# Kernel tuning notes

Hardware: AMD Instinct MI355X
Metric: run time of the kernel (lower is better)

## Reference

```python
import jax, jax.numpy as jnp
import numpy as np

LEAKY_SLOPE = 0.2
LN_EPS = 1e-5
SOFTMAX_EPS = 1e-16  # PyG softmax denominator eps


def setup_inputs() -> dict:
    key = jax.random.key(0)
    ks = jax.random.split(key, 8)
    N, E, F, H, C, ED = 100000, 1600000, 64, 8, 8, 16
    s = 1.0 / np.sqrt(F)
    return {
        "x": jax.random.normal(ks[0], (N, F), jnp.float32),
        "edge_index": jax.random.randint(ks[1], (2, E), 0, N, jnp.int32),
        "edge_attr": jax.random.normal(ks[2], (E, ED), jnp.float32),
        "W_l": jax.random.normal(ks[3], (H * C, F), jnp.float32) * s,
        "b_l": jnp.zeros((H * C,), jnp.float32),
        "W_r": jax.random.normal(ks[4], (H * C, F), jnp.float32) * s,
        "b_r": jnp.zeros((H * C,), jnp.float32),
        "W_e": jax.random.normal(ks[5], (H * C, ED), jnp.float32) * (1.0 / np.sqrt(ED)),
        "att": jax.random.normal(ks[6], (1, H, C), jnp.float32) * (1.0 / np.sqrt(C)),
        "bias": jnp.zeros((H * C,), jnp.float32),
        "gamma": jnp.ones((F,), jnp.float32),
        "beta": jnp.zeros((F,), jnp.float32),
    }


def reference(x, edge_index, edge_attr, W_l, b_l, W_r, b_r, W_e, att, bias, gamma, beta):
    N, F = x.shape
    H, C = att.shape[1], att.shape[2]
    src, dst = edge_index[0], edge_index[1]  # PyG: row0=source(j), row1=target(i)

    xl = (x @ W_l.T + b_l).reshape(N, H, C)   # lin_l -> x_j side
    xr = (x @ W_r.T + b_r).reshape(N, H, C)   # lin_r -> x_i side
    e = (edge_attr @ W_e.T).reshape(-1, H, C)  # lin_edge (no bias)

    m = jax.nn.leaky_relu(xl[src] + xr[dst] + e, LEAKY_SLOPE)  # [E,H,C]
    logits = jnp.einsum('ehc,hc->eh', m, att[0])               # [E,H]

    # per-destination segment softmax
    mx = jax.ops.segment_max(logits, dst, num_segments=N)      # [N,H]
    mx = jnp.where(jnp.isfinite(mx), mx, 0.0)                  # nodes w/o in-edges
    ex = jnp.exp(logits - mx[dst])
    denom = jax.ops.segment_sum(ex, dst, num_segments=N)
    alpha = ex / (denom[dst] + SOFTMAX_EPS)                    # [E,H]; dropout is identity in eval

    agg = jax.ops.segment_sum(alpha[:, :, None] * xl[src], dst, num_segments=N)  # [N,H,C]
    out = agg.reshape(N, H * C) + bias

    h = out + x  # residual
    mu = jnp.mean(h, axis=-1, keepdims=True)
    var = jnp.mean((h - mu) ** 2, axis=-1, keepdims=True)
    hn = (h - mu) * jax.lax.rsqrt(var + LN_EPS) * gamma + beta
    return jax.nn.relu(hn)
```

## Files before the change

kernel.cpp:

```cpp
#include <hip/hip_runtime.h>

#define LEAKY 0.2f
#define LN_EPS 1e-5f
#define SM_EPS 1e-16f
#define CAP 64
#define WPAD 68

#define BIN_SHIFT 8
#define MAXBINS   448
#define CHUNK_A   7168
#define BCAP      4608
#define EMASK     0x1FFFFF

__global__ __launch_bounds__(256) void k_node_linear(
    const float* __restrict__ x,
    const float* __restrict__ Wl,
    const float* __restrict__ bl,
    const float* __restrict__ Wr,
    const float* __restrict__ br,
    float* __restrict__ xl, float* __restrict__ xr, int N)
{
    __shared__ __align__(16) float sW[64 * WPAD];

    const int tid = threadIdx.x;
    const int side = blockIdx.x & 1;
    const float* __restrict__ W  = side ? Wr : Wl;
    const float* __restrict__ bv = side ? br : bl;
    float* __restrict__ dst      = side ? xr : xl;

    for (int i = tid; i < 4096; i += 256)
        sW[(i >> 6) * WPAD + (i & 63)] = W[i];
    __syncthreads();

    const int lane = tid & 63;
    float4 wq[16];
    #pragma unroll
    for (int q = 0; q < 16; ++q)
        wq[q] = *(const float4*)&sW[lane * WPAD + q * 4];
    const float bb = bv[lane];

    const int stream0 = (blockIdx.x >> 1) * 4 + (tid >> 6);
    const int nstream = (gridDim.x >> 1) * 4;
    for (int n = stream0; n < N; n += nstream) {
        const float4* xrow = (const float4*)(x + (long long)n * 64);
        float a = bb;
        #pragma unroll
        for (int q = 0; q < 16; ++q) {
            const float4 xv = xrow[q];
            const float4 w  = wq[q];
            a = fmaf(xv.x, w.x, fmaf(xv.y, w.y, fmaf(xv.z, w.z, fmaf(xv.w, w.w, a))));
        }
        dst[(long long)n * 64 + lane] = a;
    }
}

__global__ __launch_bounds__(256) void k_bucket(
    const int* __restrict__ ei, int* __restrict__ deg,
    int2* __restrict__ slot2, int E)
{
    const int e = blockIdx.x * 256 + threadIdx.x;
    if (e >= E) return;
    const int dst = ei[E + e];
    const int pos = atomicAdd(deg + dst, 1);
    if (pos < CAP) slot2[(long long)dst * CAP + pos] = make_int2(e, ei[e]);
}

__global__ __launch_bounds__(256) void k_binA(
    const int* __restrict__ ei,
    int* __restrict__ binCnt,
    int2* __restrict__ binArr,
    int E, int nbins)
{
    __shared__ int2 ord[CHUNK_A];
    __shared__ int cnt[MAXBINS], offs[MAXBINS], cur[MAXBINS], resB[MAXBINS];

    const int tid  = threadIdx.x;
    const int lane = tid & 63;
    const int ebase = blockIdx.x * CHUNK_A;
    const int nE = (E - ebase < CHUNK_A) ? (E - ebase) : CHUNK_A;
    const int* __restrict__ dstp = ei + E + ebase;
    const int* __restrict__ srcp = ei + ebase;

    for (int b = tid; b < MAXBINS; b += 256) { cnt[b] = 0; cur[b] = 0; }
    __syncthreads();

    for (int i = tid; i < nE; i += 256)
        atomicAdd(&cnt[dstp[i] >> BIN_SHIFT], 1);
    __syncthreads();

    if (tid < 64) {
        int carry = 0;
        #pragma unroll
        for (int seg = 0; seg < MAXBINS / 64; ++seg) {
            const int v = cnt[seg * 64 + lane];
            int s = v;
            #pragma unroll
            for (int off = 1; off < 64; off <<= 1) {
                const int t = __shfl_up(s, off, 64);
                if (lane >= off) s += t;
            }
            offs[seg * 64 + lane] = carry + s - v;
            carry += __shfl(s, 63, 64);
        }
    }
    __syncthreads();

    for (int i = tid; i < nE; i += 256) {
        const int d = dstp[i];
        const int b = d >> BIN_SHIFT;
        const int pos = atomicAdd(&cur[b], 1);
        ord[offs[b] + pos] =
            make_int2((ebase + i) | ((d & ((1 << BIN_SHIFT) - 1)) << 21), srcp[i]);
    }
    __syncthreads();

    for (int b = tid; b < nbins; b += 256) {
        const int c = cnt[b];
        resB[b] = c ? atomicAdd(&binCnt[b], c) : 0;
    }
    __syncthreads();

    const int wv = tid >> 6;
    for (int b = wv; b < nbins; b += 4) {
        const int c = cnt[b], o = offs[b], r = resB[b];
        for (int k = lane; k < c; k += 64) {
            const int kk = r + k;
            if (kk < BCAP) binArr[(long long)b * BCAP + kk] = ord[o + k];
        }
    }
}

__global__ __launch_bounds__(256) void k_binB(
    const int* __restrict__ binCnt,
    const int2* __restrict__ binArr,
    int* __restrict__ deg,
    int2* __restrict__ slot2,
    int N)
{
    __shared__ int2 ord2[BCAP];
    __shared__ int cnt2[256], offs2[256], cur2[256];

    const int b = blockIdx.x;
    const int tid  = threadIdx.x;
    const int lane = tid & 63;
    const int dst0 = b << BIN_SHIFT;
    int nb = binCnt[b];
    if (nb > BCAP) nb = BCAP;
    const int2* __restrict__ src = binArr + (long long)b * BCAP;

    cnt2[tid] = 0; cur2[tid] = 0;
    __syncthreads();

    for (int i = tid; i < nb; i += 256)
        atomicAdd(&cnt2[((unsigned)src[i].x >> 21) & 0xFF], 1);
    __syncthreads();

    if (tid < 64) {
        int carry = 0;
        #pragma unroll
        for (int seg = 0; seg < 4; ++seg) {
            const int v = cnt2[seg * 64 + lane];
            int s = v;
            #pragma unroll
            for (int off = 1; off < 64; off <<= 1) {
                const int t = __shfl_up(s, off, 64);
                if (lane >= off) s += t;
            }
            offs2[seg * 64 + lane] = carry + s - v;
            carry += __shfl(s, 63, 64);
        }
    }
    __syncthreads();

    for (int i = tid; i < nb; i += 256) {
        const int2 p = src[i];
        const int d = ((unsigned)p.x >> 21) & 0xFF;
        const int pos = atomicAdd(&cur2[d], 1);
        ord2[offs2[d] + pos] = make_int2(p.x & EMASK, p.y);
    }
    __syncthreads();

    const int nd = (N - dst0 < 256) ? (N - dst0) : 256;
    if (tid < nd) deg[dst0 + tid] = cnt2[tid];

    const int wv = tid >> 6;
    for (int d = wv; d < nd; d += 4) {
        int c = cnt2[d];
        if (c > CAP) c = CAP;
        if (lane < c) slot2[(long long)(dst0 + d) * CAP + lane] = ord2[offs2[d] + lane];
    }
}

__global__ __launch_bounds__(256) void k_gather(
    const float* __restrict__ ea,
    const float* __restrict__ We,
    const float* __restrict__ att,
    const float* __restrict__ xl, const float* __restrict__ xr,
    const int* __restrict__ deg, const int2* __restrict__ slot2,
    const float* __restrict__ x,
    const float* __restrict__ bias, const float* __restrict__ gamma,
    const float* __restrict__ beta,
    float* __restrict__ out, int N)
{
    const int lane = threadIdx.x & 63;
    const int n = blockIdx.x * 4 + (threadIdx.x >> 6);
    if (n >= N) return;

    const float4* w4 = (const float4*)(We + lane * 16);
    const float4 w0 = w4[0], w1 = w4[1], w2 = w4[2], w3 = w4[3];
    const float attv = att[lane];
    const float xrv = xr[(long long)n * 64 + lane];

    const int d = min(deg[n], CAP);

    int veid = 0, vsrc = 0;
    if (lane < d) {
        const int2 es = slot2[(long long)n * CAP + lane];
        veid = es.x;
        vsrc = es.y;
    }

    float acc = 0.f;
    float ns  = 0.f;

    float xlA = 0.f, xlB = 0.f;
    float4 a0, a1, a2, a3, b0, b1, b2, b3;
    a0 = a1 = a2 = a3 = b0 = b1 = b2 = b3 = make_float4(0.f, 0.f, 0.f, 0.f);

#define FETCH(j, XLV, E0, E1, E2, E3) do {                       \
        const int s_ = __shfl(vsrc, (j), 64);                    \
        const int e_ = __shfl(veid, (j), 64);                    \
        XLV = xl[(long long)s_ * 64 + lane];                     \
        const float4* p_ = (const float4*)(ea + (long long)e_ * 16); \
        E0 = p_[0]; E1 = p_[1]; E2 = p_[2]; E3 = p_[3];          \
    } while (0)

#define COMPUTE(XLV, E0, E1, E2, E3) do {                        \
        float ep = E0.x*w0.x + E0.y*w0.y + E0.z*w0.z + E0.w*w0.w \
                 + E1.x*w1.x + E1.y*w1.y + E1.z*w1.z + E1.w*w1.w \
                 + E2.x*w2.x + E2.y*w2.y + E2.z*w2.z + E2.w*w2.w \
                 + E3.x*w3.x + E3.y*w3.y + E3.z*w3.z + E3.w*w3.w;\
        float m = XLV + xrv + ep;                                \
        m = (m > 0.f) ? m : LEAKY * m;           \
        float p = m * attv;                                      \
        p += __shfl_xor(p, 1, 64);                               \
        p += __shfl_xor(p, 2, 64);                               \
        p += __shfl_xor(p, 4, 64);                               \
        const float ex = __expf(p);                              \
        ns  += ex;                                               \
        acc = fmaf(ex, XLV, acc);                                \
    } while (0)

    if (d > 0) FETCH(0, xlA, a0, a1, a2, a3);
    if (d > 1) FETCH(1, xlB, b0, b1, b2, b3);

    for (int i = 0; i < d; i += 2) {
        COMPUTE(xlA, a0, a1, a2, a3);
        if (i + 2 < d) FETCH(i + 2, xlA, a0, a1, a2, a3);
        if (i + 1 < d) {
            COMPUTE(xlB, b0, b1, b2, b3);
            if (i + 3 < d) FETCH(i + 3, xlB, b0, b1, b2, b3);
        }
    }
#undef FETCH
#undef COMPUTE

    const float a = acc / (ns + SM_EPS);
    const float hv = a + bias[lane] + x[(long long)n * 64 + lane];

    float s = hv;
    #pragma unroll
    for (int off = 32; off; off >>= 1) s += __shfl_xor(s, off, 64);
    const float mu = s * (1.f / 64.f);
    const float dd = hv - mu;
    float v = dd * dd;
    #pragma unroll
    for (int off = 32; off; off >>= 1) v += __shfl_xor(v, off, 64);
    const float var = v * (1.f / 64.f);

    float hn = dd * rsqrtf(var + LN_EPS) * gamma[lane] + beta[lane];
    out[(long long)n * 64 + lane] = (hn > 0.f) ? hn : 0.f;
}

extern "C" void kernel_launch(void* const* d_in, const int* in_sizes, int n_in,
                              void* d_out, int out_size, void* d_ws, size_t ws_size,
                              hipStream_t stream) {
    (void)n_in; (void)out_size;

    const float* x     = (const float*)d_in[0];
    const int*   ei    = (const int*)d_in[1];
    const float* ea    = (const float*)d_in[2];
    const float* Wl    = (const float*)d_in[3];
    const float* bl    = (const float*)d_in[4];
    const float* Wr    = (const float*)d_in[5];
    const float* br    = (const float*)d_in[6];
    const float* We    = (const float*)d_in[7];
    const float* att   = (const float*)d_in[8];
    const float* bias  = (const float*)d_in[9];
    const float* gamma = (const float*)d_in[10];
    const float* beta  = (const float*)d_in[11];

    const int N = in_sizes[0] / 64;
    const int E = in_sizes[1] / 2;
    const int nbins = (N + (1 << BIN_SHIFT) - 1) >> BIN_SHIFT;

    float* w = (float*)d_ws;
    float* xl   = w;                      w += (size_t)N * 64;
    float* xr   = w;                      w += (size_t)N * 64;
    int* deg    = (int*)w;
    int* binCnt = deg + N;
    int2* slot2 = (int2*)(binCnt + MAXBINS);
    int2* binArr = slot2 + (size_t)N * CAP;
    const size_t needed = ((char*)(binArr + (size_t)nbins * BCAP)) - (char*)d_ws;

    float* out = (float*)d_out;

    const bool binned = (nbins <= MAXBINS) && (E <= (1 << 21)) &&
                        (ws_size >= needed);

    hipMemsetAsync(deg, 0, ((size_t)N + MAXBINS) * sizeof(int), stream);

    k_node_linear<<<2048, 256, 0, stream>>>(x, Wl, bl, Wr, br, xl, xr, N);

    if (binned) {
        const int nbA = (E + CHUNK_A - 1) / CHUNK_A;
        k_binA<<<nbA, 256, 0, stream>>>(ei, binCnt, binArr, E, nbins);
        k_binB<<<nbins, 256, 0, stream>>>(binCnt, binArr, deg, slot2, N);
    } else {
        k_bucket<<<(E + 255) / 256, 256, 0, stream>>>(ei, deg, slot2, E);
    }

    k_gather<<<(N + 3) / 4, 256, 0, stream>>>(
        ea, We, att, xl, xr, deg, slot2, x, bias, gamma, beta, out, N);
}
```

Measured before the change: 645.9 us.

## Process four nodes per wavefront in gather and flatten bin scatter loop

```diff
diff --git a/kernel.cpp b/kernel.cpp
--- a/kernel.cpp
+++ b/kernel.cpp
@@ -8,9 +8,10 @@
 
 #define BIN_SHIFT 8
 #define MAXBINS   448
-#define CHUNK_A   7168
+#define CHUNK_A   5632
 #define BCAP      4608
 #define EMASK     0x1FFFFF
+#define NPW       4
 
 __global__ __launch_bounds__(256) void k_node_linear(
     const float* __restrict__ x,
@@ -72,6 +73,7 @@
     int E, int nbins)
 {
     __shared__ int2 ord[CHUNK_A];
+    __shared__ unsigned short ordBin[CHUNK_A];
     __shared__ int cnt[MAXBINS], offs[MAXBINS], cur[MAXBINS], resB[MAXBINS];
 
     const int tid  = threadIdx.x;
@@ -109,8 +111,9 @@
         const int d = dstp[i];
         const int b = d >> BIN_SHIFT;
         const int pos = atomicAdd(&cur[b], 1);
-        ord[offs[b] + pos] =
-            make_int2((ebase + i) | ((d & ((1 << BIN_SHIFT) - 1)) << 21), srcp[i]);
+        const int at = offs[b] + pos;
+        ord[at] = make_int2((ebase + i) | ((d & ((1 << BIN_SHIFT) - 1)) << 21), srcp[i]);
+        ordBin[at] = (unsigned short)b;
     }
     __syncthreads();
 
@@ -120,13 +123,10 @@
     }
     __syncthreads();
 
-    const int wv = tid >> 6;
-    for (int b = wv; b < nbins; b += 4) {
-        const int c = cnt[b], o = offs[b], r = resB[b];
-        for (int k = lane; k < c; k += 64) {
-            const int kk = r + k;
-            if (kk < BCAP) binArr[(long long)b * BCAP + kk] = ord[o + k];
-        }
+    for (int i = tid; i < nE; i += 256) {
+        const int b = ordBin[i];
+        const int k = resB[b] + (i - offs[b]);
+        if (k < BCAP) binArr[(long long)b * BCAP + k] = ord[i];
     }
 }
 
@@ -203,33 +203,41 @@
     float* __restrict__ out, int N)
 {
     const int lane = threadIdx.x & 63;
-    const int n = blockIdx.x * 4 + (threadIdx.x >> 6);
-    if (n >= N) return;
+    const int wid  = blockIdx.x * 4 + (threadIdx.x >> 6);
+    const int n0   = wid * NPW;
+    if (n0 >= N) return;
 
     const float4* w4 = (const float4*)(We + lane * 16);
     const float4 w0 = w4[0], w1 = w4[1], w2 = w4[2], w3 = w4[3];
-    const float attv = att[lane];
-    const float xrv = xr[(long long)n * 64 + lane];
-
-    const int d = min(deg[n], CAP);
-
-    int veid = 0, vsrc = 0;
-    if (lane < d) {
-        const int2 es = slot2[(long long)n * CAP + lane];
-        veid = es.x;
-        vsrc = es.y;
-    }
-
-    float acc = 0.f;
-    float ns  = 0.f;
-
-    float xlA = 0.f, xlB = 0.f;
-    float4 a0, a1, a2, a3, b0, b1, b2, b3;
-    a0 = a1 = a2 = a3 = b0 = b1 = b2 = b3 = make_float4(0.f, 0.f, 0.f, 0.f);
-
-#define FETCH(j, XLV, E0, E1, E2, E3) do {                       \
-        const int s_ = __shfl(vsrc, (j), 64);                    \
-        const int e_ = __shfl(veid, (j), 64);                    \
+    const float attv  = att[lane];
+    const float biasv = bias[lane];
+    const float gv    = gamma[lane];
+    const float bev   = beta[lane];
+
+    for (int j = 0; j < NPW; ++j) {
+        const int n = n0 + j;
+        if (n >= N) break;
+
+        const float xrv = xr[(long long)n * 64 + lane];
+        const int d = min(deg[n], CAP);
+
+        int veid = 0, vsrc = 0;
+        if (lane < d) {
+            const int2 es = slot2[(long long)n * CAP + lane];
+            veid = es.x;
+            vsrc = es.y;
+        }
+
+        float acc = 0.f;
+        float ns  = 0.f;
+
+        float xlA = 0.f, xlB = 0.f;
+        float4 a0, a1, a2, a3, b0, b1, b2, b3;
+        a0 = a1 = a2 = a3 = b0 = b1 = b2 = b3 = make_float4(0.f, 0.f, 0.f, 0.f);
+
+#define FETCH(jj, XLV, E0, E1, E2, E3) do {                      \
+        const int s_ = __shfl(vsrc, (jj), 64);                   \
+        const int e_ = __shfl(veid, (jj), 64);                   \
         XLV = xl[(long long)s_ * 64 + lane];                     \
         const float4* p_ = (const float4*)(ea + (long long)e_ * 16); \
         E0 = p_[0]; E1 = p_[1]; E2 = p_[2]; E3 = p_[3];          \
@@ -251,35 +259,36 @@
         acc = fmaf(ex, XLV, acc);                                \
     } while (0)
 
-    if (d > 0) FETCH(0, xlA, a0, a1, a2, a3);
-    if (d > 1) FETCH(1, xlB, b0, b1, b2, b3);
-
-    for (int i = 0; i < d; i += 2) {
-        COMPUTE(xlA, a0, a1, a2, a3);
-        if (i + 2 < d) FETCH(i + 2, xlA, a0, a1, a2, a3);
-        if (i + 1 < d) {
-            COMPUTE(xlB, b0, b1, b2, b3);
-            if (i + 3 < d) FETCH(i + 3, xlB, b0, b1, b2, b3);
-        }
-    }
+        if (d > 0) FETCH(0, xlA, a0, a1, a2, a3);
+        if (d > 1) FETCH(1, xlB, b0, b1, b2, b3);
+
+        for (int i = 0; i < d; i += 2) {
+            COMPUTE(xlA, a0, a1, a2, a3);
+            if (i + 2 < d) FETCH(i + 2, xlA, a0, a1, a2, a3);
+            if (i + 1 < d) {
+                COMPUTE(xlB, b0, b1, b2, b3);
+                if (i + 3 < d) FETCH(i + 3, xlB, b0, b1, b2, b3);
+            }
+        }
 #undef FETCH
 #undef COMPUTE
 
-    const float a = acc / (ns + SM_EPS);
-    const float hv = a + bias[lane] + x[(long long)n * 64 + lane];
-
-    float s = hv;
-    #pragma unroll
-    for (int off = 32; off; off >>= 1) s += __shfl_xor(s, off, 64);
-    const float mu = s * (1.f / 64.f);
-    const float dd = hv - mu;
-    float v = dd * dd;
-    #pragma unroll
-    for (int off = 32; off; off >>= 1) v += __shfl_xor(v, off, 64);
-    const float var = v * (1.f / 64.f);
-
-    float hn = dd * rsqrtf(var + LN_EPS) * gamma[lane] + beta[lane];
-    out[(long long)n * 64 + lane] = (hn > 0.f) ? hn : 0.f;
+        const float a = acc / (ns + SM_EPS);
+        const float hv = a + biasv + x[(long long)n * 64 + lane];
+
+        float s = hv;
+        #pragma unroll
+        for (int off = 32; off; off >>= 1) s += __shfl_xor(s, off, 64);
+        const float mu = s * (1.f / 64.f);
+        const float dd = hv - mu;
+        float v = dd * dd;
+        #pragma unroll
+        for (int off = 32; off; off >>= 1) v += __shfl_xor(v, off, 64);
+        const float var = v * (1.f / 64.f);
+
+        float hn = dd * rsqrtf(var + LN_EPS) * gv + bev;
+        out[(long long)n * 64 + lane] = (hn > 0.f) ? hn : 0.f;
+    }
 }
 
 extern "C" void kernel_launch(void* const* d_in, const int* in_sizes, int n_in,
@@ -330,6 +339,6 @@
         k_bucket<<<(E + 255) / 256, 256, 0, stream>>>(ei, deg, slot2, E);
     }
 
-    k_gather<<<(N + 3) / 4, 256, 0, stream>>>(
+    k_gather<<<(N + 16 * 1 - 1) / 16, 256, 0, stream>>>(
         ea, We, att, xl, xr, deg, slot2, x, bias, gamma, beta, out, N);
 }
```

Measured after the change: 620.8 us. -3.9%, faster.
